# Kernel tuning notes

Hardware: AMD Instinct MI355X
Metric: run time of the kernel (lower is better)

## Reference

```python
import jax, jax.numpy as jnp
import numpy as np


def _ccl_min_prop(mask):
    """8-connected connected-component labeling via min-index propagation.

    mask: [B,H,W] int, 1 = foreground. Returns labels [B,H,W] where every
    foreground pixel carries the minimum linear index of its 8-connected
    component and background pixels carry the sentinel S = H*W.
    Label identities differ from the original serial bwlabel, but the
    partition into components is identical, which is all downstream math uses.
    """
    B, H, W = mask.shape
    S = H * W
    idx = jnp.arange(S, dtype=jnp.int32).reshape(1, H, W)
    fg = mask > 0
    lab0 = jnp.where(fg, idx, jnp.int32(S))

    def neigh_min(lab):
        p = jnp.pad(lab, ((0, 0), (1, 1), (1, 1)), constant_values=S)
        m = lab
        for dj in (-1, 0, 1):
            for dk in (-1, 0, 1):
                if dj == 0 and dk == 0:
                    continue
                m = jnp.minimum(m, p[:, 1 + dj:1 + dj + H, 1 + dk:1 + dk + W])
        return jnp.where(fg, m, jnp.int32(S))

    def cond(carry):
        _, changed = carry
        return changed

    def body(carry):
        lab, _ = carry
        new = neigh_min(lab)
        return new, jnp.any(new != lab)

    lab, _ = jax.lax.while_loop(cond, body, (lab0, jnp.bool_(True)))
    return lab


def setup_inputs() -> dict:
    key = jax.random.key(0)
    k1, k2, k3 = jax.random.split(key, 3)
    B, C, H, W = 64, 256, 64, 64
    K, P = 5, 3  # num_classes, local_proto
    feat_map = jax.random.normal(k1, (B, C, H, W), dtype=jnp.float32)
    mask = jax.random.randint(k2, (B, H, W), 0, 2, dtype=jnp.int32)
    SFC = jax.random.uniform(k3, (K, P, C), dtype=jnp.float32)
    return {"feat_map": feat_map, "mask": mask, "SFC": SFC}


def reference(feat_map, mask, SFC):
    B, C, H, W = feat_map.shape
    S = H * W
    eps = 1e-12

    # 1) connected-component labels (background -> sentinel S)
    lab = _ccl_min_prop(mask)  # [B,H,W] in [0, S]

    # 2) per-component masked mean pooling (segment reduce)
    seg = (lab + jnp.arange(B, dtype=jnp.int32)[:, None, None] * (S + 1)).reshape(-1)
    fx = feat_map.transpose(0, 2, 3, 1).reshape(B * S, C)  # [B*H*W, C]
    sums = jax.ops.segment_sum(fx, seg, num_segments=B * (S + 1))
    cnts = jax.ops.segment_sum(jnp.ones((B * S,), feat_map.dtype), seg,
                               num_segments=B * (S + 1))
    sums = sums.reshape(B, S + 1, C)[:, :S]   # drop background slot (start_lab=1)
    cnts = cnts.reshape(B, S + 1)[:, :S]
    valid = cnts > 0                          # which segment ids are real components
    means = sums / jnp.maximum(cnts, 1.0)[..., None]  # [B,S,C]

    # 3) cosine match against SFC prototypes
    xn = means / jnp.maximum(jnp.linalg.norm(means, axis=-1, keepdims=True), eps)
    sn = SFC / jnp.maximum(jnp.linalg.norm(SFC, axis=-1, keepdims=True), eps)
    sim = jnp.einsum('kpc,bsc->bkps', sn, xn)  # cosine similarity
    mx = jnp.max(sim, axis=2)                  # max over local prototypes -> [B,K,S]
    vm = valid[:, None, :].astype(mx.dtype)
    score = jnp.sum(mx * vm, axis=-1) / jnp.maximum(jnp.sum(vm, axis=-1), 1.0)
    return score  # [B, num_classes]
```

## Files before the change

### kernel.cpp

```cpp
#include <hip/hip_runtime.h>

#define TPB     256
#define CCL_TPB 1024
#define S_PIX   4096
#define NCH     256
#define NB      64
#define MAXC    1024
#define KP      15

__global__ __launch_bounds__(TPB) void sfc_norm_kernel(
    const float* __restrict__ sfc, float* __restrict__ sn)
{
    int t = threadIdx.x;
    int kp = t >> 4, l = t & 15;
    if (kp < KP) {
        const float* v = sfc + kp * NCH;
        float s = 0.f;
        for (int c = l; c < NCH; c += 16) { float x = v[c]; s += x * x; }
        #pragma unroll
        for (int m = 8; m >= 1; m >>= 1) s += __shfl_xor(s, m, 16);
        float inv = 1.f / fmaxf(sqrtf(s), 1e-12f);
        for (int c = l; c < NCH; c += 16) sn[kp * NCH + c] = v[c] * inv;
    }
}

__device__ __forceinline__ int uf_find(int* lab, int x) {
    int p = lab[x];
    while (p != lab[p]) p = lab[p];
    return p;
}
__device__ __forceinline__ void uf_merge(int* lab, int a, int b) {
    for (;;) {
        a = uf_find(lab, a);
        b = uf_find(lab, b);
        if (a == b) return;
        int mx = a > b ? a : b;
        int mn = a > b ? b : a;
        int old = atomicMin(&lab[mx], mn);
        if (old == mx) return;
        a = old; b = mn;
    }
}

__global__ __launch_bounds__(CCL_TPB) void ccl_uf_kernel(
    const int* __restrict__ mask, int* __restrict__ cid,
    int* __restrict__ ncomp, int* __restrict__ gcomp)
{
    __shared__ int lab[S_PIX];
    __shared__ int sz[S_PIX];
    __shared__ int rid[S_PIX];
    __shared__ int cnt, gpack;
    const int b = blockIdx.x, t = threadIdx.x;
    const int* mb = mask + b * S_PIX;

    for (int i = t; i < S_PIX; i += CCL_TPB) {
        lab[i] = (mb[i] > 0) ? i : -1;
        sz[i] = 0;
    }
    if (t == 0) { cnt = 0; gpack = -1; }
    __syncthreads();

    for (int i = t; i < S_PIX; i += CCL_TPB) {
        if (lab[i] < 0) continue;
        int x = i & 63;
        if (x > 0 && lab[i - 1] >= 0) uf_merge(lab, i, i - 1);
        if (i >= 64) {
            if (lab[i - 64] >= 0) uf_merge(lab, i, i - 64);
            if (x > 0  && lab[i - 65] >= 0) uf_merge(lab, i, i - 65);
            if (x < 63 && lab[i - 63] >= 0) uf_merge(lab, i, i - 63);
        }
    }
    __syncthreads();

    for (int i = t; i < S_PIX; i += CCL_TPB) {
        if (lab[i] >= 0) {
            int r = uf_find(lab, i);
            lab[i] = r;
            atomicAdd(&sz[r], 1);
        }
    }
    __syncthreads();

    for (int i = t; i < S_PIX; i += CCL_TPB) {
        if (lab[i] == i) {
            int d = atomicAdd(&cnt, 1);
            rid[i] = d;
            atomicMax(&gpack, (sz[i] << 13) | d);
        }
    }
    __syncthreads();

    int* co = cid + b * S_PIX;
    for (int i = t; i < S_PIX; i += CCL_TPB) {
        int l = lab[i];
        co[i] = (l >= 0) ? rid[l] : -1;
    }
    if (t == 0) { ncomp[b] = cnt; gcomp[b] = (gpack >= 0) ? (gpack & 8191) : -1; }
}

__global__ __launch_bounds__(TPB) void accum_kernel(
    const float* __restrict__ feat, const float* __restrict__ sn,
    const int* __restrict__ cid, const int* __restrict__ ncomp,
    const int* __restrict__ gcomp, float* __restrict__ pdots)
{
    __shared__ __align__(16) int scid[S_PIX];
    __shared__ float acc[8 * MAXC];
    __shared__ float snc[KP * 8];
    const int b  = blockIdx.y;
    const int c0 = blockIdx.x * 8;
    const int t  = threadIdx.x;

    {
        const int4* src = reinterpret_cast<const int4*>(cid + b * S_PIX);
        int4* dst = reinterpret_cast<int4*>(scid);
        for (int i = t; i < S_PIX / 4; i += TPB) dst[i] = src[i];
    }
    for (int i = t; i < 8 * MAXC; i += TPB) acc[i] = 0.f;
    if (t < KP * 8) {
        int kp = t >> 3, h = t & 7;
        snc[t] = sn[kp * NCH + c0 + h];
    }
    __syncthreads();

    const int gc = gcomp[b];
    const int wave = t >> 6, lane = t & 63;
    const int chl0 = wave * 2;
    const float* fb  = feat + (size_t)b * NCH * S_PIX;
    const float* fr0 = fb + (size_t)(c0 + chl0) * S_PIX;
    const float* fr1 = fr0 + S_PIX;
    float* a0 = acc + chl0 * MAXC;
    float* a1 = a0 + MAXC;
    float g0 = 0.f, g1 = 0.f;

    auto flush0 = [&](int c, float r) {
        if (c >= 0) { if (c == gc) g0 += r; else atomicAdd(&a0[c], r); }
    };
    auto flush1 = [&](int c, float r) {
        if (c >= 0) { if (c == gc) g1 += r; else atomicAdd(&a1[c], r); }
    };

    for (int base = 0; base < S_PIX; base += 256) {
        const int p = base + lane * 4;
        int4 q = *reinterpret_cast<const int4*>(&scid[p]);
        if ((q.x & q.y & q.z & q.w) == -1) continue;
        float4 v0 = *reinterpret_cast<const float4*>(&fr0[p]);
        float4 v1 = *reinterpret_cast<const float4*>(&fr1[p]);
        {
            int cur = q.x; float rs = v0.x;
            if (q.y == cur) rs += v0.y; else { flush0(cur, rs); cur = q.y; rs = v0.y; }
            if (q.z == cur) rs += v0.z; else { flush0(cur, rs); cur = q.z; rs = v0.z; }
            if (q.w == cur) rs += v0.w; else { flush0(cur, rs); cur = q.w; rs = v0.w; }
            flush0(cur, rs);
        }
        {
            int cur = q.x; float rs = v1.x;
            if (q.y == cur) rs += v1.y; else { flush1(cur, rs); cur = q.y; rs = v1.y; }
            if (q.z == cur) rs += v1.z; else { flush1(cur, rs); cur = q.z; rs = v1.z; }
            if (q.w == cur) rs += v1.w; else { flush1(cur, rs); cur = q.w; rs = v1.w; }
            flush1(cur, rs);
        }
    }
    #pragma unroll
    for (int m = 32; m >= 1; m >>= 1) {
        g0 += __shfl_xor(g0, m);
        g1 += __shfl_xor(g1, m);
    }
    if (lane == 0 && gc >= 0) { a0[gc] = g0; a1[gc] = g1; }
    __syncthreads();

    const int n = ncomp[b];
    for (int j = t; j < n; j += TPB) {
        float s[8]; float n2 = 0.f;
        #pragma unroll
        for (int h = 0; h < 8; ++h) { float x = acc[h * MAXC + j]; s[h] = x; n2 += x * x; }
        float* dst = pdots + (size_t)(b * MAXC + j) * 16;
        #pragma unroll
        for (int kp = 0; kp < KP; ++kp) {
            float d = 0.f;
            #pragma unroll
            for (int h = 0; h < 8; ++h) d += snc[kp * 8 + h] * s[h];
            atomicAdd(&dst[kp], d);
        }
        atomicAdd(&dst[KP], n2);
    }
}

__global__ __launch_bounds__(TPB) void score_kernel(
    const float* __restrict__ pdots, const int* __restrict__ ncomp,
    float* __restrict__ out)
{
    __shared__ float red[5][TPB];
    const int b = blockIdx.x, t = threadIdx.x;
    const int n = ncomp[b];
    float ak[5] = {0.f, 0.f, 0.f, 0.f, 0.f};
    for (int j = t; j < n; j += TPB) {
        const float* d = pdots + (size_t)(b * MAXC + j) * 16;
        float4 d0 = *(const float4*)(d + 0);
        float4 d1 = *(const float4*)(d + 4);
        float4 d2 = *(const float4*)(d + 8);
        float4 d3 = *(const float4*)(d + 12);
        float inv = 1.f / fmaxf(sqrtf(d3.w), 1e-12f);
        ak[0] += fmaxf(fmaxf(d0.x, d0.y), d0.z) * inv;
        ak[1] += fmaxf(fmaxf(d0.w, d1.x), d1.y) * inv;
        ak[2] += fmaxf(fmaxf(d1.z, d1.w), d2.x) * inv;
        ak[3] += fmaxf(fmaxf(d2.y, d2.z), d2.w) * inv;
        ak[4] += fmaxf(fmaxf(d3.x, d3.y), d3.z) * inv;
    }
    #pragma unroll
    for (int k = 0; k < 5; ++k) red[k][t] = ak[k];
    __syncthreads();
    for (int s = TPB / 2; s > 0; s >>= 1) {
        if (t < s) {
            #pragma unroll
            for (int k = 0; k < 5; ++k) red[k][t] += red[k][t + s];
        }
        __syncthreads();
    }
    if (t < 5) out[b * 5 + t] = red[t][0] / (float)max(n, 1);
}

extern "C" void kernel_launch(void* const* d_in, const int* in_sizes, int n_in,
                              void* d_out, int out_size, void* d_ws, size_t ws_size,
                              hipStream_t stream)
{
    const float* feat = (const float*)d_in[0];
    const int*   mask = (const int*)d_in[1];
    const float* sfc  = (const float*)d_in[2];
    float* out = (float*)d_out;
    char* ws = (char*)d_ws;

    int*   cid   = (int*)ws;
    int*   ncomp = (int*)(ws + 1048576);
    int*   gcomp = (int*)(ws + 1048576 + 1024);
    float* sn    = (float*)(ws + 1048576 + 2048);
    float* pdots = (float*)(ws + 1048576 + 2048 + 15360);

    hipMemsetAsync(pdots, 0, (size_t)NB * MAXC * 16 * 4, stream);
    sfc_norm_kernel<<<1, TPB, 0, stream>>>(sfc, sn);
    ccl_uf_kernel<<<NB, CCL_TPB, 0, stream>>>(mask, cid, ncomp, gcomp);
    accum_kernel<<<dim3(32, NB), TPB, 0, stream>>>(feat, sn, cid, ncomp, gcomp, pdots);
    score_kernel<<<NB, TPB, 0, stream>>>(pdots, ncomp, out);
}
```

Before: 495.7 us.

## Rework CCL merge rules and accumulate four channels per block with direct loads

```diff
diff --git a/kernel.cpp b/kernel.cpp
--- a/kernel.cpp
+++ b/kernel.cpp
@@ -7,6 +7,8 @@
 #define NB      64
 #define MAXC    1024
 #define KP      15
+#define CPB     4
+#define NCHUNK  (NCH / CPB)
 
 __global__ __launch_bounds__(TPB) void sfc_norm_kernel(
     const float* __restrict__ sfc, float* __restrict__ sn)
@@ -26,8 +28,12 @@
 
 __device__ __forceinline__ int uf_find(int* lab, int x) {
     int p = lab[x];
-    while (p != lab[p]) p = lab[p];
-    return p;
+    for (;;) {
+        int gp = lab[p];
+        if (gp == p) return p;
+        atomicMin(&lab[x], gp);
+        x = p; p = gp;
+    }
 }
 __device__ __forceinline__ void uf_merge(int* lab, int a, int b) {
     for (;;) {
@@ -51,23 +57,38 @@
     __shared__ int rid[S_PIX];
     __shared__ int cnt, gpack;
     const int b = blockIdx.x, t = threadIdx.x;
+    const int wave = t >> 6, lane = t & 63;
     const int* mb = mask + b * S_PIX;
 
-    for (int i = t; i < S_PIX; i += CCL_TPB) {
-        lab[i] = (mb[i] > 0) ? i : -1;
-        sz[i] = 0;
+    for (int r = wave; r < 64; r += 16) {
+        bool fg = mb[r * 64 + lane] > 0;
+        unsigned long long bits = __ballot(fg);
+        int labv = -1;
+        if (fg) {
+            unsigned long long zeros = ~bits;
+            unsigned long long below = (lane == 63) ? zeros
+                                     : (zeros & ((1ull << (lane + 1)) - 1));
+            int start = (below == 0) ? 0 : (64 - __clzll(below));
+            labv = r * 64 + start;
+        }
+        lab[r * 64 + lane] = labv;
+        sz[r * 64 + lane] = 0;
     }
     if (t == 0) { cnt = 0; gpack = -1; }
     __syncthreads();
 
-    for (int i = t; i < S_PIX; i += CCL_TPB) {
+    for (int i = t + 64; i < S_PIX; i += CCL_TPB) {
         if (lab[i] < 0) continue;
         int x = i & 63;
-        if (x > 0 && lab[i - 1] >= 0) uf_merge(lab, i, i - 1);
-        if (i >= 64) {
-            if (lab[i - 64] >= 0) uf_merge(lab, i, i - 64);
-            if (x > 0  && lab[i - 65] >= 0) uf_merge(lab, i, i - 65);
-            if (x < 63 && lab[i - 63] >= 0) uf_merge(lab, i, i - 63);
+        bool nf  = lab[i - 64] >= 0;
+        bool nwf = x > 0  && lab[i - 65] >= 0;
+        bool nef = x < 63 && lab[i - 63] >= 0;
+        bool wf  = x > 0  && lab[i - 1]  >= 0;
+        if (nf) {
+            if (!(wf && nwf)) uf_merge(lab, i, i - 64);
+        } else {
+            if (nwf) uf_merge(lab, i, i - 65);
+            if (nef) uf_merge(lab, i, i - 63);
         }
     }
     __syncthreads();
@@ -98,87 +119,83 @@
     if (t == 0) { ncomp[b] = cnt; gcomp[b] = (gpack >= 0) ? (gpack & 8191) : -1; }
 }
 
-__global__ __launch_bounds__(TPB) void accum_kernel(
+__global__ __launch_bounds__(TPB, 4) void accum_kernel(
     const float* __restrict__ feat, const float* __restrict__ sn,
     const int* __restrict__ cid, const int* __restrict__ ncomp,
     const int* __restrict__ gcomp, float* __restrict__ pdots)
 {
-    __shared__ __align__(16) int scid[S_PIX];
-    __shared__ float acc[8 * MAXC];
-    __shared__ float snc[KP * 8];
+    __shared__ float acc[CPB * MAXC];
+    __shared__ float snc[KP * CPB];
     const int b  = blockIdx.y;
-    const int c0 = blockIdx.x * 8;
+    const int c0 = blockIdx.x * CPB;
     const int t  = threadIdx.x;
 
-    {
-        const int4* src = reinterpret_cast<const int4*>(cid + b * S_PIX);
-        int4* dst = reinterpret_cast<int4*>(scid);
-        for (int i = t; i < S_PIX / 4; i += TPB) dst[i] = src[i];
-    }
-    for (int i = t; i < 8 * MAXC; i += TPB) acc[i] = 0.f;
-    if (t < KP * 8) {
-        int kp = t >> 3, h = t & 7;
-        snc[t] = sn[kp * NCH + c0 + h];
-    }
+    for (int i = t; i < CPB * MAXC; i += TPB) acc[i] = 0.f;
+    if (t < KP * CPB) snc[t] = sn[(t >> 2) * NCH + c0 + (t & 3)];
     __syncthreads();
 
     const int gc = gcomp[b];
     const int wave = t >> 6, lane = t & 63;
-    const int chl0 = wave * 2;
-    const float* fb  = feat + (size_t)b * NCH * S_PIX;
-    const float* fr0 = fb + (size_t)(c0 + chl0) * S_PIX;
-    const float* fr1 = fr0 + S_PIX;
-    float* a0 = acc + chl0 * MAXC;
-    float* a1 = a0 + MAXC;
-    float g0 = 0.f, g1 = 0.f;
-
-    auto flush0 = [&](int c, float r) {
-        if (c >= 0) { if (c == gc) g0 += r; else atomicAdd(&a0[c], r); }
+    const int4*  cb = reinterpret_cast<const int4*>(cid + b * S_PIX);
+    const float4* f4 = reinterpret_cast<const float4*>(
+        feat + (size_t)b * NCH * S_PIX + (size_t)c0 * S_PIX);
+    float g[CPB] = {0.f, 0.f, 0.f, 0.f};
+
+    auto pe = [&](int c, float e0, float e1, float e2, float e3) {
+        if (c == gc) { g[0] += e0; g[1] += e1; g[2] += e2; g[3] += e3; }
+        else if (c >= 0) {
+            atomicAdd(&acc[c], e0);
+            atomicAdd(&acc[MAXC + c], e1);
+            atomicAdd(&acc[2 * MAXC + c], e2);
+            atomicAdd(&acc[3 * MAXC + c], e3);
+        }
     };
-    auto flush1 = [&](int c, float r) {
-        if (c >= 0) { if (c == gc) g1 += r; else atomicAdd(&a1[c], r); }
+    auto proc = [&](const int4& q, const float4 (&v)[CPB]) {
+        if ((q.x & q.y & q.z & q.w) == -1) return;
+        pe(q.x, v[0].x, v[1].x, v[2].x, v[3].x);
+        pe(q.y, v[0].y, v[1].y, v[2].y, v[3].y);
+        pe(q.z, v[0].z, v[1].z, v[2].z, v[3].z);
+        pe(q.w, v[0].w, v[1].w, v[2].w, v[3].w);
     };
 
-    for (int base = 0; base < S_PIX; base += 256) {
-        const int p = base + lane * 4;
-        int4 q = *reinterpret_cast<const int4*>(&scid[p]);
-        if ((q.x & q.y & q.z & q.w) == -1) continue;
-        float4 v0 = *reinterpret_cast<const float4*>(&fr0[p]);
-        float4 v1 = *reinterpret_cast<const float4*>(&fr1[p]);
-        {
-            int cur = q.x; float rs = v0.x;
-            if (q.y == cur) rs += v0.y; else { flush0(cur, rs); cur = q.y; rs = v0.y; }
-            if (q.z == cur) rs += v0.z; else { flush0(cur, rs); cur = q.z; rs = v0.z; }
-            if (q.w == cur) rs += v0.w; else { flush0(cur, rs); cur = q.w; rs = v0.w; }
-            flush0(cur, rs);
-        }
-        {
-            int cur = q.x; float rs = v1.x;
-            if (q.y == cur) rs += v1.y; else { flush1(cur, rs); cur = q.y; rs = v1.y; }
-            if (q.z == cur) rs += v1.z; else { flush1(cur, rs); cur = q.z; rs = v1.z; }
-            if (q.w == cur) rs += v1.w; else { flush1(cur, rs); cur = q.w; rs = v1.w; }
-            flush1(cur, rs);
-        }
-    }
+    const int base = wave * 256;
+    #pragma unroll
+    for (int it = 0; it < 4; it += 2) {
+        const int qi0 = base + it * 64 + lane;
+        const int qi1 = qi0 + 64;
+        const int4 q0 = cb[qi0];
+        const int4 q1 = cb[qi1];
+        float4 v0[CPB], v1[CPB];
+        #pragma unroll
+        for (int h = 0; h < CPB; ++h) v0[h] = f4[h * (S_PIX / 4) + qi0];
+        #pragma unroll
+        for (int h = 0; h < CPB; ++h) v1[h] = f4[h * (S_PIX / 4) + qi1];
+        proc(q0, v0);
+        proc(q1, v1);
+    }
+
     #pragma unroll
     for (int m = 32; m >= 1; m >>= 1) {
-        g0 += __shfl_xor(g0, m);
-        g1 += __shfl_xor(g1, m);
-    }
-    if (lane == 0 && gc >= 0) { a0[gc] = g0; a1[gc] = g1; }
+        #pragma unroll
+        for (int h = 0; h < CPB; ++h) g[h] += __shfl_xor(g[h], m);
+    }
+    if (lane == 0 && gc >= 0) {
+        #pragma unroll
+        for (int h = 0; h < CPB; ++h) atomicAdd(&acc[h * MAXC + gc], g[h]);
+    }
     __syncthreads();
 
     const int n = ncomp[b];
     for (int j = t; j < n; j += TPB) {
-        float s[8]; float n2 = 0.f;
-        #pragma unroll
-        for (int h = 0; h < 8; ++h) { float x = acc[h * MAXC + j]; s[h] = x; n2 += x * x; }
+        float s[CPB]; float n2 = 0.f;
+        #pragma unroll
+        for (int h = 0; h < CPB; ++h) { float x = acc[h * MAXC + j]; s[h] = x; n2 += x * x; }
         float* dst = pdots + (size_t)(b * MAXC + j) * 16;
         #pragma unroll
         for (int kp = 0; kp < KP; ++kp) {
             float d = 0.f;
             #pragma unroll
-            for (int h = 0; h < 8; ++h) d += snc[kp * 8 + h] * s[h];
+            for (int h = 0; h < CPB; ++h) d += snc[kp * CPB + h] * s[h];
             atomicAdd(&dst[kp], d);
         }
         atomicAdd(&dst[KP], n2);
@@ -238,6 +255,6 @@
     hipMemsetAsync(pdots, 0, (size_t)NB * MAXC * 16 * 4, stream);
     sfc_norm_kernel<<<1, TPB, 0, stream>>>(sfc, sn);
     ccl_uf_kernel<<<NB, CCL_TPB, 0, stream>>>(mask, cid, ncomp, gcomp);
-    accum_kernel<<<dim3(32, NB), TPB, 0, stream>>>(feat, sn, cid, ncomp, gcomp, pdots);
+    accum_kernel<<<dim3(NCHUNK, NB), TPB, 0, stream>>>(feat, sn, cid, ncomp, gcomp, pdots);
     score_kernel<<<NB, TPB, 0, stream>>>(pdots, ncomp, out);
 }
```

After: 587.9 us. 1.19x slower.
